# Optimization experiments

Hardware: AMD Instinct MI355X
Metric: run time of the kernel (lower is better)

## Reference

```python
import math
import jax, jax.numpy as jnp
import numpy as np

FACTOR = 1  # init factor; top_k = max(1, int(FACTOR * log(L)))


def setup_inputs() -> dict:
    key = jax.random.key(0)
    kq, kk, kv = jax.random.split(key, 3)
    B, L, H, E = 8, 4096, 8, 64
    queries = jax.random.normal(kq, (B, L, H, E), dtype=jnp.float32)
    keys = jax.random.normal(kk, (B, L, H, E), dtype=jnp.float32)
    values = jax.random.normal(kv, (B, L, H, E), dtype=jnp.float32)
    return {"queries": queries, "keys": keys, "values": values}


def reference(queries, keys, values):
    # queries/keys: [B, L, H, E], values: [B, L, H, D] (L == S so no padding branch)
    B, L, H, E = queries.shape
    q = jnp.transpose(queries, (0, 2, 3, 1))  # [B, H, E, L]
    k = jnp.transpose(keys, (0, 2, 3, 1))
    v = jnp.transpose(values, (0, 2, 3, 1))   # [B, H, D, L]

    # FFT-based circular cross-correlation along time axis
    qf = jnp.fft.rfft(q, axis=-1)
    kf = jnp.fft.rfft(k, axis=-1)
    corr = jnp.fft.irfft(qf * jnp.conj(kf), n=L, axis=-1)  # [B, H, E, L]

    # Inference-time delay aggregation (eval path of the module)
    top_k = max(1, int(FACTOR * math.log(L)))
    mean_corr = corr.mean(axis=(1, 2))                      # [B, L]
    w_top, idx_top = jax.lax.top_k(mean_corr, top_k)        # [B, K]
    w = jax.nn.softmax(w_top, axis=-1)                      # [B, K]

    # circular shift: out[..., t] = sum_i w_i * v[..., (t + delay_i) mod L]
    t = jnp.arange(L)
    idx = (t[None, None, :] + idx_top[:, :, None]) % L      # [B, K, L]
    gathered = jnp.take_along_axis(
        v[:, None], idx[:, :, None, None, :], axis=-1
    )                                                       # [B, K, H, D, L]
    agg = jnp.einsum('bkhdl,bk->bhdl', gathered, w)         # [B, H, D, L]
    return jnp.transpose(agg, (0, 3, 1, 2))                 # [B, L, H, D]
```

## Files before the change

### kernel.cpp

```cpp
#include <hip/hip_runtime.h>
#include <math.h>


namespace {
constexpr int LEN  = 4096;
constexpr int NCH  = 512;
constexpr int NB   = 8;
constexpr int KTOP = 8;
constexpr int TPB  = 256;
constexpr int CPB  = 8;
constexpr int GPB  = NCH / CPB;
constexpr size_t SF_BYTES = (size_t)NB * LEN * 2 * sizeof(float);
constexpr size_t WI_BYTES = (size_t)NB * KTOP * sizeof(float);
constexpr size_t ZT_OFF   = SF_BYTES + 2 * WI_BYTES;
constexpr size_t ZT_BYTES = (size_t)NB * NCH * LEN * 2 * sizeof(float);
constexpr int PADN = LEN + (LEN >> 4);
}

#define PD(i) ((i) + ((i) >> 4))

__device__ __forceinline__ float2 cmul(float2 a, float2 b) {
  return make_float2(a.x * b.x - a.y * b.y, a.x * b.y + a.y * b.x);
}

__device__ __forceinline__ void gload_lds16(const void* g, void* l) {
  __builtin_amdgcn_global_load_lds(
      (const __attribute__((address_space(1))) void*)g,
      (__attribute__((address_space(3))) void*)l, 16, 0, 0);
}

#define LGKM_BAR()                                          \
  do {                                                      \
    asm volatile("s_waitcnt lgkmcnt(0)" ::: "memory");      \
    __builtin_amdgcn_s_barrier();                           \
  } while (0)
#define FULL_BAR()                                          \
  do {                                                      \
    asm volatile("s_waitcnt vmcnt(0) lgkmcnt(0)" ::: "memory"); \
    __builtin_amdgcn_s_barrier();                           \
  } while (0)

__device__ __forceinline__ void dft16(const float2* __restrict__ a,
                                      float2* __restrict__ b) {
  const float C1 = 0.92387953251128674f;
  const float S1 = 0.38268343236508978f;
  const float R2 = 0.70710678118654752f;
  float2 c[4][4];
  #pragma unroll
  for (int r0 = 0; r0 < 4; ++r0) {
    const float2 x0 = a[r0], x1 = a[4 + r0], x2 = a[8 + r0], x3 = a[12 + r0];
    const float2 s02 = make_float2(x0.x + x2.x, x0.y + x2.y);
    const float2 d02 = make_float2(x0.x - x2.x, x0.y - x2.y);
    const float2 s13 = make_float2(x1.x + x3.x, x1.y + x3.y);
    const float2 d13 = make_float2(x1.x - x3.x, x1.y - x3.y);
    c[r0][0] = make_float2(s02.x + s13.x, s02.y + s13.y);
    c[r0][2] = make_float2(s02.x - s13.x, s02.y - s13.y);
    c[r0][1] = make_float2(d02.x + d13.y, d02.y - d13.x);
    c[r0][3] = make_float2(d02.x - d13.y, d02.y + d13.x);
  }
  #pragma unroll
  for (int k0 = 0; k0 < 4; ++k0) {
    float2 t0 = c[0][k0], t1 = c[1][k0], t2 = c[2][k0], t3 = c[3][k0];
    if (k0 == 1) {
      t1 = cmul(t1, make_float2(C1, -S1));
      t2 = cmul(t2, make_float2(R2, -R2));
      t3 = cmul(t3, make_float2(S1, -C1));
    } else if (k0 == 2) {
      t1 = cmul(t1, make_float2(R2, -R2));
      t2 = make_float2(t2.y, -t2.x);
      t3 = cmul(t3, make_float2(-R2, -R2));
    } else if (k0 == 3) {
      t1 = cmul(t1, make_float2(S1, -C1));
      t2 = cmul(t2, make_float2(-R2, -R2));
      t3 = cmul(t3, make_float2(-C1, S1));
    }
    const float2 s02 = make_float2(t0.x + t2.x, t0.y + t2.y);
    const float2 d02 = make_float2(t0.x - t2.x, t0.y - t2.y);
    const float2 s13 = make_float2(t1.x + t3.x, t1.y + t3.y);
    const float2 d13 = make_float2(t1.x - t3.x, t1.y - t3.y);
    b[k0]      = make_float2(s02.x + s13.x, s02.y + s13.y);
    b[k0 + 8]  = make_float2(s02.x - s13.x, s02.y - s13.y);
    b[k0 + 4]  = make_float2(d02.x + d13.y, d02.y - d13.x);
    b[k0 + 12] = make_float2(d02.x - d13.y, d02.y + d13.x);
  }
}

__device__ __forceinline__ void fft4096_ip(float2* __restrict__ buf, int tid)
{
  float2 a[16], b[16];
  const float NEG2PI_N = -6.283185307179586f / 4096.0f;
  {
    #pragma unroll
    for (int r = 0; r < 16; ++r) a[r] = buf[PD(tid + 256 * r)];
    dft16(a, b);
    float sn, cs;
    __sincosf((float)tid * NEG2PI_N, &sn, &cs);
    const float2 w1 = make_float2(cs, sn);
    __syncthreads();
    float2 w = make_float2(1.f, 0.f);
    #pragma unroll
    for (int k = 0; k < 16; ++k) {
      buf[PD(16 * tid + k)] = cmul(b[k], w);
      w = cmul(w, w1);
    }
  }
  __syncthreads();
  {
    const int q = tid & 15, p = tid >> 4;
    #pragma unroll
    for (int r = 0; r < 16; ++r) a[r] = buf[PD(tid + 256 * r)];
    dft16(a, b);
    float sn, cs;
    __sincosf((float)(16 * p) * NEG2PI_N, &sn, &cs);
    const float2 w1 = make_float2(cs, sn);
    __syncthreads();
    float2 w = make_float2(1.f, 0.f);
    const int ob = q + 256 * p;
    #pragma unroll
    for (int k = 0; k < 16; ++k) {
      buf[PD(ob + 16 * k)] = cmul(b[k], w);
      w = cmul(w, w1);
    }
  }
  __syncthreads();
  {
    #pragma unroll
    for (int r = 0; r < 16; ++r) a[r] = buf[PD(tid + 256 * r)];
    dft16(a, b);
    __syncthreads();
    #pragma unroll
    for (int k = 0; k < 16; ++k) buf[PD(tid + 256 * k)] = b[k];
  }
  __syncthreads();
}

__global__ __launch_bounds__(TPB) void k_transpose(
    const float* __restrict__ qg, const float* __restrict__ kg,
    float2* __restrict__ zt)
{
  __shared__ float2 tile[64 * 65];
  const int bt  = blockIdx.x;
  const int b   = bt >> 9;
  const int t0  = ((bt >> 3) & 63) * 64;
  const int c0  = (bt & 7) * 64;
  const int tid = threadIdx.x;
  const size_t base = (size_t)b * LEN * NCH;

  #pragma unroll
  for (int r = 0; r < 16; ++r) {
    const int idx  = r * TPB + tid;
    const int ch_l = idx & 63;
    const int t_l  = idx >> 6;
    const size_t g = base + (size_t)(t0 + t_l) * NCH + (c0 + ch_l);
    tile[t_l * 65 + ch_l] = make_float2(qg[g], kg[g]);
  }
  __syncthreads();
  #pragma unroll
  for (int r = 0; r < 16; ++r) {
    const int idx  = r * TPB + tid;
    const int t_l  = idx & 63;
    const int ch_l = idx >> 6;
    zt[((size_t)b * NCH + (c0 + ch_l)) * LEN + (t0 + t_l)] =
        tile[t_l * 65 + ch_l];
  }
}

__device__ __forceinline__ void spec_acc(const float2* __restrict__ buf,
                                         int tid, float2* __restrict__ acc)
{
  #pragma unroll
  for (int r = 0; r < 16; ++r) {
    const int f = tid + 256 * r;
    const float2 A = buf[PD(f)];
    float2 Bv = buf[PD((LEN - f) & (LEN - 1))];
    Bv.y = -Bv.y;
    const float Sx = A.x + Bv.x, Sy = A.y + Bv.y;
    const float Dx = A.x - Bv.x, Dy = -(A.y - Bv.y);
    const float Mx = Sx * Dx - Sy * Dy;
    const float My = Sx * Dy + Sy * Dx;
    acc[r].x += -0.25f * My;
    acc[r].y +=  0.25f * Mx;
  }
}

__global__ __launch_bounds__(TPB) void k_fft_corr(
    const float2* __restrict__ zt,
    float* __restrict__ Sf)
{
  __shared__ float2 bufA[PADN];
  __shared__ float2 bufS[LEN];
  const int tid  = threadIdx.x;
  const int lane = tid & 63;
  const int wv   = tid >> 6;
  const int b    = blockIdx.x / GPB;
  const int g    = blockIdx.x % GPB;
  const float2* base = zt + ((size_t)b * NCH + g * CPB) * LEN;

  float2 acc[16];
  #pragma unroll
  for (int r = 0; r < 16; ++r) acc[r] = make_float2(0.f, 0.f);

  {
    const char* gs = (const char*)base + (size_t)wv * 8192 + (size_t)lane * 16;
    char* ls = (char*)bufS + wv * 8192;
    #pragma unroll
    for (int i = 0; i < 8; ++i)
      gload_lds16(gs + i * 1024, ls + i * 1024);
  }
  FULL_BAR();

  const float NEG2PI_N = -6.283185307179586f / 4096.0f;
  for (int cc = 0; cc < CPB; ++cc) {
    float2 a[16], bb[16];
    float sn, cs;
    #pragma unroll
    for (int r = 0; r < 16; ++r) a[r] = bufS[tid + 256 * r];
    LGKM_BAR();
    if (cc + 1 < CPB) {
      const char* gs = (const char*)(base + (size_t)(cc + 1) * LEN)
                       + (size_t)wv * 8192 + (size_t)lane * 16;
      char* ls = (char*)bufS + wv * 8192;
      #pragma unroll
      for (int i = 0; i < 8; ++i)
        gload_lds16(gs + i * 1024, ls + i * 1024);
    }
    dft16(a, bb);
    __sincosf((float)tid * NEG2PI_N, &sn, &cs);
    {
      const float2 w1 = make_float2(cs, sn);
      float2 w = make_float2(1.f, 0.f);
      #pragma unroll
      for (int k = 0; k < 16; ++k) {
        bufA[PD(16 * tid + k)] = cmul(bb[k], w);
        w = cmul(w, w1);
      }
    }
    LGKM_BAR();
    #pragma unroll
    for (int r = 0; r < 16; ++r) a[r] = bufA[PD(tid + 256 * r)];
    LGKM_BAR();
    dft16(a, bb);
    {
      const int qq = tid & 15, p = tid >> 4;
      __sincosf((float)(16 * p) * NEG2PI_N, &sn, &cs);
      const float2 w1 = make_float2(cs, sn);
      float2 w = make_float2(1.f, 0.f);
      const int ob = qq + 256 * p;
      #pragma unroll
      for (int k = 0; k < 16; ++k) {
        bufA[PD(ob + 16 * k)] = cmul(bb[k], w);
        w = cmul(w, w1);
      }
    }
    LGKM_BAR();
    #pragma unroll
    for (int r = 0; r < 16; ++r) a[r] = bufA[PD(tid + 256 * r)];
    LGKM_BAR();
    dft16(a, bb);
    #pragma unroll
    for (int k = 0; k < 16; ++k) bufA[PD(tid + 256 * k)] = bb[k];
    LGKM_BAR();
    spec_acc(bufA, tid, acc);
    FULL_BAR();
  }
  float* dstp = Sf + (size_t)b * LEN * 2;
  #pragma unroll
  for (int r = 0; r < 16; ++r) {
    const int f = tid + 256 * r;
    atomicAdd(&dstp[2 * f],     acc[r].x);
    atomicAdd(&dstp[2 * f + 1], acc[r].y);
  }
}

__global__ __launch_bounds__(TPB) void k_fft_corr_strided(
    const float* __restrict__ qg, const float* __restrict__ kg,
    float* __restrict__ Sf)
{
  __shared__ float2 buf[PADN];
  const int tid = threadIdx.x;
  const int b   = blockIdx.x / GPB;
  const int g   = blockIdx.x % GPB;
  const int ch0 = g * CPB;

  float2 acc[16];
  #pragma unroll
  for (int r = 0; r < 16; ++r) acc[r] = make_float2(0.f, 0.f);

  const size_t base = (size_t)b * LEN * NCH;
  for (int cc = 0; cc < CPB; ++cc) {
    const int ch = ch0 + cc;
    #pragma unroll
    for (int r = 0; r < 16; ++r) {
      const int t = tid + 256 * r;
      const size_t idx = base + (size_t)t * NCH + ch;
      buf[PD(t)] = make_float2(qg[idx], kg[idx]);
    }
    __syncthreads();
    fft4096_ip(buf, tid);
    spec_acc(buf, tid, acc);
    __syncthreads();
  }
  float* dstp = Sf + (size_t)b * LEN * 2;
  #pragma unroll
  for (int r = 0; r < 16; ++r) {
    const int f = tid + 256 * r;
    atomicAdd(&dstp[2 * f],     acc[r].x);
    atomicAdd(&dstp[2 * f + 1], acc[r].y);
  }
}

__global__ __launch_bounds__(TPB) void k_ifft_topk(
    const float* __restrict__ Sf,
    float* __restrict__ wout, int* __restrict__ iout)
{
  __shared__ float2 buf[PADN];
  __shared__ float swv[4];
  __shared__ int   swi[4];
  __shared__ int   gsel;
  __shared__ float topv[KTOP];
  __shared__ int   topi[KTOP];
  const int tid = threadIdx.x;
  const int b   = blockIdx.x;

  const float2* srcp = (const float2*)Sf + (size_t)b * LEN;
  #pragma unroll
  for (int r = 0; r < 16; ++r) {
    const int f = tid + 256 * r;
    const float2 s = srcp[f];
    buf[PD(f)] = make_float2(s.x, -s.y);
  }
  __syncthreads();
  fft4096_ip(buf, tid);

  const float scale = 1.0f / (4096.0f * 512.0f);
  float rv[16];
  #pragma unroll
  for (int r = 0; r < 16; ++r) rv[r] = buf[PD(tid + 256 * r)].x * scale;

  const int lane = tid & 63, wv = tid >> 6;
  for (int it = 0; it < KTOP; ++it) {
    float best = -INFINITY;
    int   bi   = 0x7fffffff;
    #pragma unroll
    for (int r = 0; r < 16; ++r) {
      if (rv[r] > best) { best = rv[r]; bi = tid + 256 * r; }
    }
    #pragma unroll
    for (int off = 32; off > 0; off >>= 1) {
      const float ov = __shfl_xor(best, off);
      const int   oi = __shfl_xor(bi, off);
      if (ov > best || (ov == best && oi < bi)) { best = ov; bi = oi; }
    }
    if (lane == 0) { swv[wv] = best; swi[wv] = bi; }
    __syncthreads();
    if (tid == 0) {
      float gv = swv[0]; int gi = swi[0];
      for (int w2 = 1; w2 < 4; ++w2)
        if (swv[w2] > gv || (swv[w2] == gv && swi[w2] < gi)) {
          gv = swv[w2]; gi = swi[w2];
        }
      topv[it] = gv; topi[it] = gi; gsel = gi;
    }
    __syncthreads();
    const int gi = gsel;
    if ((gi & 255) == tid) {
      const int rr = gi >> 8;
      #pragma unroll
      for (int r = 0; r < 16; ++r)
        if (r == rr) rv[r] = -INFINITY;
    }
  }
  if (tid == 0) {
    const float m = topv[0];
    float e[KTOP], den = 0.f;
    #pragma unroll
    for (int i = 0; i < KTOP; ++i) { e[i] = expf(topv[i] - m); den += e[i]; }
    #pragma unroll
    for (int i = 0; i < KTOP; ++i) {
      wout[b * KTOP + i] = e[i] / den;
      iout[b * KTOP + i] = topi[i];
    }
  }
}

__global__ __launch_bounds__(256) void k_gather(
    const float4* __restrict__ v, const float* __restrict__ wk,
    const int* __restrict__ ik, float4* __restrict__ out)
{
  __shared__ float sw[KTOP];
  __shared__ int   sidx[KTOP];
  const int b  = blockIdx.x >> 11;
  const int tp = blockIdx.x & 2047;
  if (threadIdx.x < KTOP) {
    sw[threadIdx.x]   = wk[b * KTOP + threadIdx.x];
    sidx[threadIdx.x] = ik[b * KTOP + threadIdx.x];
  }
  __syncthreads();
  const int t = tp * 2 + (threadIdx.x >> 7);
  const int c = threadIdx.x & 127;
  const size_t vbase = (size_t)b * LEN * 128;
  float4 acc = make_float4(0.f, 0.f, 0.f, 0.f);
  #pragma unroll
  for (int i = 0; i < KTOP; ++i) {
    const int st = (t + sidx[i]) & (LEN - 1);
    const float4 x = v[vbase + (size_t)st * 128 + c];
    acc.x += sw[i] * x.x; acc.y += sw[i] * x.y;
    acc.z += sw[i] * x.z; acc.w += sw[i] * x.w;
  }
  out[vbase + (size_t)t * 128 + c] = acc;
}

extern "C" void kernel_launch(void* const* d_in, const int* in_sizes, int n_in,
                              void* d_out, int out_size, void* d_ws, size_t ws_size,
                              hipStream_t stream) {
  const float* q = (const float*)d_in[0];
  const float* k = (const float*)d_in[1];
  const float* v = (const float*)d_in[2];

  float*  Sf = (float*)d_ws;
  float*  wk = (float*)((char*)d_ws + SF_BYTES);
  int*    ik = (int*)((char*)d_ws + SF_BYTES + WI_BYTES);
  float2* zt = (float2*)((char*)d_ws + ZT_OFF);

  hipMemsetAsync(d_ws, 0, SF_BYTES, stream);
  if (ws_size >= ZT_OFF + ZT_BYTES) {
    k_transpose<<<NB * 64 * 8, TPB, 0, stream>>>(q, k, zt);
    k_fft_corr<<<NB * GPB, TPB, 0, stream>>>(zt, Sf);
  } else {
    k_fft_corr_strided<<<NB * GPB, TPB, 0, stream>>>(q, k, Sf);
  }
  k_ifft_topk<<<NB, TPB, 0, stream>>>(Sf, wk, ik);
  k_gather<<<NB * 2048, 256, 0, stream>>>((const float4*)v, wk, ik,
                                          (float4*)d_out);
}
```

Measured before the change: 362.1 us.

## Prefetch FFT inputs into registers instead of LDS and halve channels per block

The FFT-correlation kernel stops staging the next channel in a second LDS buffer via global_load_lds and instead loads it directly into registers, issued after the first DFT stage so the load overlaps later stages. This removes the 32 KB staging buffer, which should raise occupancy, but adds register pressure. Channels per block drop from 8 to 4, doubling the grid and the atomic adds. The gather kernel's block index is remapped so batch varies fastest, interleaving batches across consecutive blocks.

```diff
diff --git a/kernel.cpp b/kernel.cpp
--- a/kernel.cpp
+++ b/kernel.cpp
@@ -8,7 +8,7 @@
 constexpr int NB   = 8;
 constexpr int KTOP = 8;
 constexpr int TPB  = 256;
-constexpr int CPB  = 8;
+constexpr int CPB  = 4;
 constexpr int GPB  = NCH / CPB;
 constexpr size_t SF_BYTES = (size_t)NB * LEN * 2 * sizeof(float);
 constexpr size_t WI_BYTES = (size_t)NB * KTOP * sizeof(float);
@@ -23,20 +23,9 @@
   return make_float2(a.x * b.x - a.y * b.y, a.x * b.y + a.y * b.x);
 }
 
-__device__ __forceinline__ void gload_lds16(const void* g, void* l) {
-  __builtin_amdgcn_global_load_lds(
-      (const __attribute__((address_space(1))) void*)g,
-      (__attribute__((address_space(3))) void*)l, 16, 0, 0);
-}
-
 #define LGKM_BAR()                                          \
   do {                                                      \
     asm volatile("s_waitcnt lgkmcnt(0)" ::: "memory");      \
-    __builtin_amdgcn_s_barrier();                           \
-  } while (0)
-#define FULL_BAR()                                          \
-  do {                                                      \
-    asm volatile("s_waitcnt vmcnt(0) lgkmcnt(0)" ::: "memory"); \
     __builtin_amdgcn_s_barrier();                           \
   } while (0)
 
@@ -188,42 +177,24 @@
     float* __restrict__ Sf)
 {
   __shared__ float2 bufA[PADN];
-  __shared__ float2 bufS[LEN];
-  const int tid  = threadIdx.x;
-  const int lane = tid & 63;
-  const int wv   = tid >> 6;
-  const int b    = blockIdx.x / GPB;
-  const int g    = blockIdx.x % GPB;
+  const int tid = threadIdx.x;
+  const int b   = blockIdx.x / GPB;
+  const int g   = blockIdx.x % GPB;
   const float2* base = zt + ((size_t)b * NCH + g * CPB) * LEN;
 
   float2 acc[16];
   #pragma unroll
   for (int r = 0; r < 16; ++r) acc[r] = make_float2(0.f, 0.f);
 
-  {
-    const char* gs = (const char*)base + (size_t)wv * 8192 + (size_t)lane * 16;
-    char* ls = (char*)bufS + wv * 8192;
-    #pragma unroll
-    for (int i = 0; i < 8; ++i)
-      gload_lds16(gs + i * 1024, ls + i * 1024);
-  }
-  FULL_BAR();
-
   const float NEG2PI_N = -6.283185307179586f / 4096.0f;
+
+  float2 a[16];
+  #pragma unroll
+  for (int r = 0; r < 16; ++r) a[r] = base[tid + 256 * r];
+
   for (int cc = 0; cc < CPB; ++cc) {
-    float2 a[16], bb[16];
+    float2 bb[16], t16[16];
     float sn, cs;
-    #pragma unroll
-    for (int r = 0; r < 16; ++r) a[r] = bufS[tid + 256 * r];
-    LGKM_BAR();
-    if (cc + 1 < CPB) {
-      const char* gs = (const char*)(base + (size_t)(cc + 1) * LEN)
-                       + (size_t)wv * 8192 + (size_t)lane * 16;
-      char* ls = (char*)bufS + wv * 8192;
-      #pragma unroll
-      for (int i = 0; i < 8; ++i)
-        gload_lds16(gs + i * 1024, ls + i * 1024);
-    }
     dft16(a, bb);
     __sincosf((float)tid * NEG2PI_N, &sn, &cs);
     {
@@ -235,17 +206,21 @@
         w = cmul(w, w1);
       }
     }
-    LGKM_BAR();
-    #pragma unroll
-    for (int r = 0; r < 16; ++r) a[r] = bufA[PD(tid + 256 * r)];
-    LGKM_BAR();
-    dft16(a, bb);
+    if (cc + 1 < CPB) {
+      const float2* nsrc = base + (size_t)(cc + 1) * LEN;
+      #pragma unroll
+      for (int r = 0; r < 16; ++r) a[r] = nsrc[tid + 256 * r];
+    }
+    LGKM_BAR();
+    #pragma unroll
+    for (int r = 0; r < 16; ++r) t16[r] = bufA[PD(tid + 256 * r)];
+    LGKM_BAR();
+    dft16(t16, bb);
+    __sincosf((float)(16 * (tid >> 4)) * NEG2PI_N, &sn, &cs);
     {
-      const int qq = tid & 15, p = tid >> 4;
-      __sincosf((float)(16 * p) * NEG2PI_N, &sn, &cs);
       const float2 w1 = make_float2(cs, sn);
       float2 w = make_float2(1.f, 0.f);
-      const int ob = qq + 256 * p;
+      const int ob = (tid & 15) + 256 * (tid >> 4);
       #pragma unroll
       for (int k = 0; k < 16; ++k) {
         bufA[PD(ob + 16 * k)] = cmul(bb[k], w);
@@ -254,14 +229,14 @@
     }
     LGKM_BAR();
     #pragma unroll
-    for (int r = 0; r < 16; ++r) a[r] = bufA[PD(tid + 256 * r)];
-    LGKM_BAR();
-    dft16(a, bb);
+    for (int r = 0; r < 16; ++r) t16[r] = bufA[PD(tid + 256 * r)];
+    LGKM_BAR();
+    dft16(t16, bb);
     #pragma unroll
     for (int k = 0; k < 16; ++k) bufA[PD(tid + 256 * k)] = bb[k];
     LGKM_BAR();
     spec_acc(bufA, tid, acc);
-    FULL_BAR();
+    LGKM_BAR();
   }
   float* dstp = Sf + (size_t)b * LEN * 2;
   #pragma unroll
@@ -389,8 +364,8 @@
 {
   __shared__ float sw[KTOP];
   __shared__ int   sidx[KTOP];
-  const int b  = blockIdx.x >> 11;
-  const int tp = blockIdx.x & 2047;
+  const int b  = blockIdx.x & 7;
+  const int tp = blockIdx.x >> 3;
   if (threadIdx.x < KTOP) {
     sw[threadIdx.x]   = wk[b * KTOP + threadIdx.x];
     sidx[threadIdx.x] = ik[b * KTOP + threadIdx.x];
```

Measured after the change: 371.3 us. 2.5% more time.
